# Performance work log

Measured on AMD Instinct MI355X. Metric: run time of the kernel, lower is better.

Reference implementation:

```python
import jax, jax.numpy as jnp
import numpy as np

N_BITS = 8
IN_FEATURES = 2048
OUT_FEATURES = 512
BATCH = 8
THRESHOLD = 0.5


def setup_inputs() -> dict:
    key = jax.random.key(0)
    kx, kw = jax.random.split(key)
    x = jax.random.uniform(kx, (BATCH, IN_FEATURES), dtype=jnp.float32)
    # nn.init.normal_(weight, mean=0.5, std=1.0) then clamp_(0, 1)
    weight = 0.5 + jax.random.normal(kw, (IN_FEATURES, OUT_FEATURES * N_BITS), dtype=jnp.float32)
    weight = jnp.clip(weight, 0.0, 1.0)
    return {"x": x, "weight": weight}


def _carry_save_adder(addends):
    # addends: [M, F, n_bits] -> reduce over F via full-adder chain.
    # Bit index 0 = LSB; carry shifts one position toward MSB each step.
    M, F, nb = addends.shape
    a_seq = jnp.transpose(addends, (1, 0, 2))  # [F, M, nb]
    init = (jnp.zeros((M, nb), addends.dtype), jnp.zeros((M, nb), addends.dtype))

    def step(state, a):
        s, c = state
        t = s + a + c
        half = jnp.floor(t * 0.5)          # carry bit (zero-gradient)
        sum_b = t - 2.0 * half             # t mod 2 (identity gradient w.r.t. t)
        c_next = jnp.pad(half[:, :-1], ((0, 0), (1, 0)))  # shift-left: LSB carry-in = 0
        return (sum_b, c_next), None

    (s, c), _ = jax.lax.scan(step, init, a_seq)
    return s, c


def reference(x, weight):
    # STE binarization of the weights (forward value = hard bits)
    w = jnp.clip(weight, 0.0, 1.0)
    hard = w + jax.lax.stop_gradient((w >= THRESHOLD).astype(w.dtype) - w)
    # [B, F, 1] * [1, F, O*nb] -> [B, F, O*nb]
    ff = x[:, :, None] * hard[None, :, :]
    B, F, _ = ff.shape
    O = ff.shape[-1] // N_BITS
    # split(n_bits, dim=-1) + stack(dim=-3) + reshape -> [B*O, F, n_bits]
    stacked = ff.reshape(B, F, O, N_BITS).transpose(0, 2, 1, 3).reshape(B * O, F, N_BITS)
    s, carry = _carry_save_adder(stacked)   # [B*O, nb], [B*O, nb]
    s = s.reshape(B, N_BITS * O)
    return (s, carry)
```

## Files before the change

### kernel.cpp

```cpp
#include <hip/hip_runtime.h>


#define F_DIM 2048
#define K_DIM 4096
#define B_DIM 8
#define U     16
#define NB    4

__device__ __forceinline__ float dpp_row_shr1(float v) {
    int r = __builtin_amdgcn_update_dpp(0, __float_as_int(v), 0x111, 0xf, 0xf, true);
    return __int_as_float(r);
}

__global__ __launch_bounds__(64, 1) void csa_kernel(const float* __restrict__ x,
                                                    const float* __restrict__ weight,
                                                    float* __restrict__ out) {
    const int lane = threadIdx.x;
    const int og   = blockIdx.x + 8 * blockIdx.y;
    const int b    = blockIdx.z;
    const int k    = og * 64 + lane;

    const float kmask = ((lane & 7) == 7) ? 0.0f : 1.0f;

    int zero;
    asm volatile("v_mov_b32 %0, 0" : "=v"(zero));

    const float*  wp  = weight + k;
    const float4* xp4 = (const float4*)(x + b * F_DIM) + zero;

    float  wb[NB][U];
    float4 xb[NB][U / 4];

#pragma unroll
    for (int p = 0; p < NB; ++p) {
#pragma unroll
        for (int u = 0; u < U; ++u)
            wb[p][u] = wp[(p * U + u) * K_DIM];
#pragma unroll
        for (int q = 0; q < U / 4; ++q)
            xb[p][q] = xp4[(p * U) / 4 + q];
    }

    float s = 0.0f, c = 0.0f;

    for (int f0 = 0; f0 < F_DIM; f0 += NB * U) {
#pragma unroll
        for (int p = 0; p < NB; ++p) {
            const float* xf = (const float*)&xb[p][0];
#pragma unroll
            for (int u = 0; u < U; ++u) {
                float a  = (wb[p][u] >= 0.5f) ? xf[u] : 0.0f;
                float uu = s + a;
                float t  = uu + c;
                bool  ge = (t >= 2.0f);
                float h  = ge ? kmask : 0.0f;
                s = ge ? (t - 2.0f) : t;
                c = dpp_row_shr1(h);
            }
            int fb = f0 + p * U + NB * U;
            int fc = (fb <= F_DIM - U) ? fb : (F_DIM - U);
#pragma unroll
            for (int u = 0; u < U; ++u)
                wb[p][u] = wp[(fc + u) * K_DIM];
#pragma unroll
            for (int q = 0; q < U / 4; ++q)
                xb[p][q] = xp4[fc / 4 + q];
        }
    }

    out[b * K_DIM + k]                 = s;
    out[B_DIM * K_DIM + b * K_DIM + k] = c;
}

extern "C" void kernel_launch(void* const* d_in, const int* in_sizes, int n_in,
                              void* d_out, int out_size, void* d_ws, size_t ws_size,
                              hipStream_t stream) {
    (void)in_sizes; (void)n_in; (void)d_ws; (void)ws_size; (void)out_size;
    const float* x      = (const float*)d_in[0];
    const float* weight = (const float*)d_in[1];
    float* out          = (float*)d_out;

    dim3 grid(8, 8, 8);
    dim3 block(64);
    csa_kernel<<<grid, block, 0, stream>>>(x, weight, out);
}
```

Before: 127.2 us.

## Pre-pack binarized weights into bitmasks in a separate kernel before the CSA scan

```diff
diff --git a/kernel.cpp b/kernel.cpp
--- a/kernel.cpp
+++ b/kernel.cpp
@@ -4,17 +4,43 @@
 #define F_DIM 2048
 #define K_DIM 4096
 #define B_DIM 8
-#define U     16
-#define NB    4
+#define G     32
+#define NG    (F_DIM / G)
+#define NB2   4
+
+#define PK_BYTES (64 * NG * 64 * 4)
 
 __device__ __forceinline__ float dpp_row_shr1(float v) {
     int r = __builtin_amdgcn_update_dpp(0, __float_as_int(v), 0x111, 0xf, 0xf, true);
     return __int_as_float(r);
 }
 
-__global__ __launch_bounds__(64, 1) void csa_kernel(const float* __restrict__ x,
-                                                    const float* __restrict__ weight,
-                                                    float* __restrict__ out) {
+__device__ __forceinline__ int sext_bit(unsigned bits, int u) {
+#if __has_builtin(__builtin_amdgcn_sbfe)
+    return __builtin_amdgcn_sbfe((int)bits, (unsigned)u, 1u);
+#else
+    return ((int)(bits << (31 - u))) >> 31;
+#endif
+}
+
+__global__ __launch_bounds__(64) void pack_kernel(const float* __restrict__ w,
+                                                  unsigned* __restrict__ pk) {
+    const int lane = threadIdx.x;
+    const int og   = blockIdx.x;
+    const int f32  = blockIdx.y;
+    const float* wp = w + og * 64 + lane;
+    unsigned bits = 0;
+#pragma unroll
+    for (int j = 0; j < 32; ++j) {
+        float wv = wp[(f32 * 32 + j) * K_DIM];
+        bits |= (wv >= 0.5f ? 1u : 0u) << j;
+    }
+    pk[(og * 64 + f32) * 64 + lane] = bits;
+}
+
+__global__ __launch_bounds__(64, 1) void csa_main(const float* __restrict__ x,
+                                                  const unsigned* __restrict__ pk,
+                                                  float* __restrict__ out) {
     const int lane = threadIdx.x;
     const int og   = blockIdx.x + 8 * blockIdx.y;
     const int b    = blockIdx.z;
@@ -25,30 +51,81 @@
     int zero;
     asm volatile("v_mov_b32 %0, 0" : "=v"(zero));
 
-    const float*  wp  = weight + k;
-    const float4* xp4 = (const float4*)(x + b * F_DIM) + zero;
+    const unsigned* bp  = pk + og * (NG * 64) + lane;
+    const float4*   xp4 = (const float4*)(x + b * F_DIM) + zero;
 
-    float  wb[NB][U];
-    float4 xb[NB][U / 4];
+    unsigned bbuf[NB2];
+    float4   xb[NB2][G / 4];
 
 #pragma unroll
-    for (int p = 0; p < NB; ++p) {
+    for (int p = 0; p < NB2; ++p) {
+        bbuf[p] = bp[p * 64];
 #pragma unroll
-        for (int u = 0; u < U; ++u)
-            wb[p][u] = wp[(p * U + u) * K_DIM];
-#pragma unroll
-        for (int q = 0; q < U / 4; ++q)
-            xb[p][q] = xp4[(p * U) / 4 + q];
+        for (int q = 0; q < G / 4; ++q)
+            xb[p][q] = xp4[p * (G / 4) + q];
     }
 
     float s = 0.0f, c = 0.0f;
 
-    for (int f0 = 0; f0 < F_DIM; f0 += NB * U) {
+    for (int g0 = 0; g0 < NG; g0 += NB2) {
 #pragma unroll
-        for (int p = 0; p < NB; ++p) {
+        for (int p = 0; p < NB2; ++p) {
+            const float*   xf   = (const float*)&xb[p][0];
+            const unsigned bits = bbuf[p];
+#pragma unroll
+            for (int u = 0; u < G; ++u) {
+                int   m  = sext_bit(bits, u);
+                float a  = __int_as_float(m & __float_as_int(xf[u]));
+                float uu = s + a;
+                float t  = uu + c;
+                bool  ge = (t >= 2.0f);
+                float h  = ge ? kmask : 0.0f;
+                s = ge ? (t - 2.0f) : t;
+                c = dpp_row_shr1(h);
+            }
+            int gb = g0 + p + NB2;
+            int gc = (gb < NG) ? gb : (NG - 1);
+            bbuf[p] = bp[gc * 64];
+#pragma unroll
+            for (int q = 0; q < G / 4; ++q)
+                xb[p][q] = xp4[gc * (G / 4) + q];
+        }
+    }
+
+    out[b * K_DIM + k]                 = s;
+    out[B_DIM * K_DIM + b * K_DIM + k] = c;
+}
+
+#define U_FB  16
+#define NB_FB 4
+__global__ __launch_bounds__(64, 1) void csa_fallback(const float* __restrict__ x,
+                                                      const float* __restrict__ weight,
+                                                      float* __restrict__ out) {
+    const int lane = threadIdx.x;
+    const int og   = blockIdx.x + 8 * blockIdx.y;
+    const int b    = blockIdx.z;
+    const int k    = og * 64 + lane;
+    const float kmask = ((lane & 7) == 7) ? 0.0f : 1.0f;
+    int zero;
+    asm volatile("v_mov_b32 %0, 0" : "=v"(zero));
+    const float*  wp  = weight + k;
+    const float4* xp4 = (const float4*)(x + b * F_DIM) + zero;
+    float  wb[NB_FB][U_FB];
+    float4 xb[NB_FB][U_FB / 4];
+#pragma unroll
+    for (int p = 0; p < NB_FB; ++p) {
+#pragma unroll
+        for (int u = 0; u < U_FB; ++u) wb[p][u] = wp[(p * U_FB + u) * K_DIM];
+#pragma unroll
+        for (int q = 0; q < U_FB / 4; ++q) xb[p][q] = xp4[(p * U_FB) / 4 + q];
+    }
+    float s = 0.0f, c = 0.0f;
+    for (int f0 = 0; f0 < F_DIM; f0 += NB_FB * U_FB) {
+#pragma unroll
+        for (int p = 0; p < NB_FB; ++p) {
             const float* xf = (const float*)&xb[p][0];
 #pragma unroll
-            for (int u = 0; u < U; ++u) {
+            for (int u = 0; u < U_FB; ++u) {
                 float a  = (wb[p][u] >= 0.5f) ? xf[u] : 0.0f;
                 float uu = s + a;
                 float t  = uu + c;
@@ -57,17 +134,14 @@
                 s = ge ? (t - 2.0f) : t;
                 c = dpp_row_shr1(h);
             }
-            int fb = f0 + p * U + NB * U;
-            int fc = (fb <= F_DIM - U) ? fb : (F_DIM - U);
+            int fb = f0 + p * U_FB + NB_FB * U_FB;
+            int fc = (fb <= F_DIM - U_FB) ? fb : (F_DIM - U_FB);
 #pragma unroll
-            for (int u = 0; u < U; ++u)
-                wb[p][u] = wp[(fc + u) * K_DIM];
+            for (int u = 0; u < U_FB; ++u) wb[p][u] = wp[(fc + u) * K_DIM];
 #pragma unroll
-            for (int q = 0; q < U / 4; ++q)
-                xb[p][q] = xp4[fc / 4 + q];
+            for (int q = 0; q < U_FB / 4; ++q) xb[p][q] = xp4[fc / 4 + q];
         }
     }
-
     out[b * K_DIM + k]                 = s;
     out[B_DIM * K_DIM + b * K_DIM + k] = c;
 }
@@ -75,12 +149,16 @@
 extern "C" void kernel_launch(void* const* d_in, const int* in_sizes, int n_in,
                               void* d_out, int out_size, void* d_ws, size_t ws_size,
                               hipStream_t stream) {
-    (void)in_sizes; (void)n_in; (void)d_ws; (void)ws_size; (void)out_size;
+    (void)in_sizes; (void)n_in; (void)out_size;
     const float* x      = (const float*)d_in[0];
     const float* weight = (const float*)d_in[1];
     float* out          = (float*)d_out;
 
-    dim3 grid(8, 8, 8);
-    dim3 block(64);
-    csa_kernel<<<grid, block, 0, stream>>>(x, weight, out);
+    if (ws_size >= (size_t)PK_BYTES && d_ws != nullptr) {
+        unsigned* pk = (unsigned*)d_ws;
+        pack_kernel<<<dim3(64, 64, 1), dim3(64), 0, stream>>>(weight, pk);
+        csa_main<<<dim3(8, 8, 8), dim3(64), 0, stream>>>(x, pk, out);
+    } else {
+        csa_fallback<<<dim3(8, 8, 8), dim3(64), 0, stream>>>(x, weight, out);
+    }
 }
```

After: 124.4 us. 1.02x faster.
